# Optimization experiments

Hardware: AMD Instinct MI355X
Metric: run time of the kernel (lower is better)

Reference implementation:

```python
import jax, jax.numpy as jnp
import numpy as np

H = 128          # input spatial size forced by hardcoded reshape (8 * 16)
BATCH = 128
BLK = 8          # block_size
SUB = 16         # out_channels (sub-frames)
WIN = 3          # window


def setup_inputs() -> dict:
    key = jax.random.key(0)
    k1, k2 = jax.random.split(key, 2)
    coded = jax.random.normal(k1, (BATCH, 1, H, H), dtype=jnp.float32)
    # Conv3d weight: [out=16*64, in/groups=1, kD=9, 1, 1]; kaiming-like scale sqrt(2/9)
    weight = jax.random.normal(k2, (SUB * BLK * BLK, 1, WIN * WIN, 1, 1), dtype=jnp.float32) * np.sqrt(2.0 / 9.0).astype(np.float32)
    bias = jnp.zeros((SUB * BLK * BLK,), dtype=jnp.float32)
    return {"coded": coded, "weight": weight, "bias": bias}


def reference(coded, weight, bias):
    N = coded.shape[0]
    # --- window_shuffle: conv with 3x3 identity filters, pad 1 == 9 shifted copies ---
    pad = jnp.pad(coded, ((0, 0), (0, 0), (1, 1), (1, 1)))  # [N,1,H+2,H+2]
    patches = jnp.stack(
        [pad[:, 0, i:i + H, j:j + H] for i in range(WIN) for j in range(WIN)],
        axis=1,
    )  # [N,9,H,H]
    # --- reverse_pixel_shuffle (space-to-depth, block 8), vectorized over the 9 channels ---
    Hs = H // BLK  # 16
    x = patches.reshape(N, WIN * WIN, Hs, BLK, Hs, BLK)
    x = x.transpose(0, 1, 3, 5, 2, 4).reshape(N, WIN * WIN, BLK * BLK, Hs, Hs)
    x = x.transpose(0, 2, 1, 3, 4)  # [N,64,9,16,16] (torch.stack dim=2 order)
    # --- depthwise Conv3d: groups=64, kernel (9,1,1) -> per-group 9-tap dot ---
    W = weight.reshape(BLK * BLK, SUB, WIN * WIN)  # [64,16,9]
    b = bias.reshape(BLK * BLK, SUB)               # [64,16]
    out = jnp.einsum('ngihw,gmi->ngmhw', x, W) + b[None, :, :, None, None]  # [N,64,16,16,16]
    # --- reshape/transpose/pixel-shuffle ---
    out = out.transpose(0, 2, 1, 3, 4).reshape(N, SUB * BLK * BLK, Hs, Hs)  # [N,1024,16,16]
    out = out.reshape(N, SUB, BLK, BLK, Hs, Hs)
    out = out.transpose(0, 1, 4, 2, 5, 3).reshape(N, SUB, H, H)  # [N,16,128,128]
    return out
```

## Files before the change

### kernel.cpp

```cpp
#include <hip/hip_runtime.h>


#define H 128
#define N_BATCH 128
#define SUB 16

__global__ void wprep_kernel(const float* __restrict__ w,
                             const float* __restrict__ bias,
                             float* __restrict__ Wt) {
    int t = blockIdx.x * blockDim.x + threadIdx.x;
    if (t >= 8 * 16 * 8) return;
    int b1 = t >> 7;
    int m  = (t >> 3) & 15;
    int j  = t & 7;
    int oc = (b1 * 8 + j) * 16 + m;
    float* dst = Wt + (b1 * 16 + m) * 80;
#pragma unroll
    for (int i = 0; i < 9; ++i) dst[j * 9 + i] = w[oc * 9 + i];
    dst[72 + j] = bias[oc];
}

__global__ __launch_bounds__(256, 8) void shiftconv_kernel(
        const float* __restrict__ x,
        const float* __restrict__ Wt,
        float* __restrict__ out) {
    int bid = blockIdx.x;
    int nlo = bid & 7;
    int q   = bid >> 3;
    int mh  = q & 1;
    int rh  = (q >> 1) & 1;
    int b1  = (q >> 2) & 7;
    int n   = ((q >> 5) << 3) | nlo;

    __shared__ float ws[8 * 80];
    {
        int t = threadIdx.x;
        if (t < 160)
            ((float4*)ws)[t] = ((const float4*)(Wt + (b1 * 16 + mh * 8) * 80))[t];
    }

    int c  = threadIdx.x & 31;
    int r8 = threadIdx.x >> 5;
    int y  = b1 + (rh << 6) + (r8 << 3);
    int x0 = c << 2;
    int h  = c & 1;

    const float* xn = x + (size_t)n * (H * H);

    float in[3][6];
#pragma unroll
    for (int dy = 0; dy < 3; ++dy) {
        int ry = y + dy - 1;
        if (ry >= 0 && ry < H) {
            const float* row = xn + ry * H + x0;
            float4 a = *(const float4*)(row);
            in[dy][1] = a.x; in[dy][2] = a.y; in[dy][3] = a.z; in[dy][4] = a.w;
            in[dy][0] = (x0 > 0)     ? row[-1] : 0.0f;
            in[dy][5] = (x0 + 4 < H) ? row[4]  : 0.0f;
        } else {
#pragma unroll
            for (int k = 0; k < 6; ++k) in[dy][k] = 0.0f;
        }
    }

    __syncthreads();

    float* outbase = out + ((size_t)(n * SUB + mh * 8)) * (H * H) + y * H + x0;

#pragma unroll
    for (int mi = 0; mi < 8; ++mi) {
        const float* wb  = ws + mi * 80;
        const float* wpp = wb + h * 36;
        float acc[4];
#pragma unroll
        for (int j = 0; j < 4; ++j) acc[j] = wb[72 + 4 * h + j];
#pragma unroll
        for (int dy = 0; dy < 3; ++dy) {
#pragma unroll
            for (int dj = 0; dj < 3; ++dj) {
#pragma unroll
                for (int j = 0; j < 4; ++j) {
                    acc[j] = fmaf(in[dy][j + dj], wpp[j * 9 + dy * 3 + dj], acc[j]);
                }
            }
        }
        *(float4*)(outbase + (size_t)mi * (H * H)) =
            make_float4(acc[0], acc[1], acc[2], acc[3]);
    }
}

extern "C" void kernel_launch(void* const* d_in, const int* in_sizes, int n_in,
                              void* d_out, int out_size, void* d_ws, size_t ws_size,
                              hipStream_t stream) {
    const float* coded  = (const float*)d_in[0];
    const float* weight = (const float*)d_in[1];
    const float* bias   = (const float*)d_in[2];
    float* out = (float*)d_out;
    float* Wt  = (float*)d_ws;

    wprep_kernel<<<4, 256, 0, stream>>>(weight, bias, Wt);
    shiftconv_kernel<<<N_BATCH * 8 * 2 * 2, 256, 0, stream>>>(coded, Wt, out);
}
```

Measured before the change: 151.2 us.

## Fuse weight prep into conv kernel and keep weights in registers

Removes the separate weight-reorder kernel and has each block gather its weights and bias from global memory into shared memory. The thread mapping changes so each warp owns one output channel and keeps its 40 weights in registers while looping over 8 rows, instead of reading weights from shared memory per channel. Horizontal halo values now come from warp shuffles rather than extra scalar loads, and outputs are written with nontemporal stores. In exchange it uses more registers (launch bounds drop to 4 blocks per SM), reloads input rows once per channel-warp, and does uncoalesced strided weight gathers in every block.

```diff
diff --git a/kernel.cpp b/kernel.cpp
--- a/kernel.cpp
+++ b/kernel.cpp
@@ -5,24 +5,12 @@
 #define N_BATCH 128
 #define SUB 16
 
-__global__ void wprep_kernel(const float* __restrict__ w,
-                             const float* __restrict__ bias,
-                             float* __restrict__ Wt) {
-    int t = blockIdx.x * blockDim.x + threadIdx.x;
-    if (t >= 8 * 16 * 8) return;
-    int b1 = t >> 7;
-    int m  = (t >> 3) & 15;
-    int j  = t & 7;
-    int oc = (b1 * 8 + j) * 16 + m;
-    float* dst = Wt + (b1 * 16 + m) * 80;
-#pragma unroll
-    for (int i = 0; i < 9; ++i) dst[j * 9 + i] = w[oc * 9 + i];
-    dst[72 + j] = bias[oc];
-}
+typedef float floatx4 __attribute__((ext_vector_type(4)));
 
-__global__ __launch_bounds__(256, 8) void shiftconv_kernel(
+__global__ __launch_bounds__(256, 4) void shiftconv_kernel(
         const float* __restrict__ x,
-        const float* __restrict__ Wt,
+        const float* __restrict__ w,
+        const float* __restrict__ bias,
         float* __restrict__ out) {
     int bid = blockIdx.x;
     int nlo = bid & 7;
@@ -32,60 +20,70 @@
     int b1  = (q >> 2) & 7;
     int n   = ((q >> 5) << 3) | nlo;
 
-    __shared__ float ws[8 * 80];
+    __shared__ float ws[8 * 2 * 40];
     {
         int t = threadIdx.x;
-        if (t < 160)
-            ((float4*)ws)[t] = ((const float4*)(Wt + (b1 * 16 + mh * 8) * 80))[t];
+        if (t < 64) {
+            int ml = t >> 3, j = t & 7;
+            int oc = b1 * 128 + j * 16 + mh * 8 + ml;
+            float* dst = ws + (ml * 2 + (j >> 2)) * 40;
+            int j4 = j & 3;
+#pragma unroll
+            for (int i = 0; i < 9; ++i) dst[j4 * 9 + i] = w[oc * 9 + i];
+            dst[36 + j4] = bias[oc];
+        }
     }
+    __syncthreads();
 
     int c  = threadIdx.x & 31;
-    int r8 = threadIdx.x >> 5;
-    int y  = b1 + (rh << 6) + (r8 << 3);
+    int mq = threadIdx.x >> 5;
+    int h  = c & 1;
     int x0 = c << 2;
-    int h  = c & 1;
 
-    const float* xn = x + (size_t)n * (H * H);
-
-    float in[3][6];
+    float wr[40];
+    {
+        const float4* wp = (const float4*)(ws + (mq * 2 + h) * 40);
 #pragma unroll
-    for (int dy = 0; dy < 3; ++dy) {
-        int ry = y + dy - 1;
-        if (ry >= 0 && ry < H) {
-            const float* row = xn + ry * H + x0;
-            float4 a = *(const float4*)(row);
-            in[dy][1] = a.x; in[dy][2] = a.y; in[dy][3] = a.z; in[dy][4] = a.w;
-            in[dy][0] = (x0 > 0)     ? row[-1] : 0.0f;
-            in[dy][5] = (x0 + 4 < H) ? row[4]  : 0.0f;
-        } else {
-#pragma unroll
-            for (int k = 0; k < 6; ++k) in[dy][k] = 0.0f;
+        for (int k = 0; k < 10; ++k) {
+            float4 v = wp[k];
+            wr[4 * k]     = v.x;
+            wr[4 * k + 1] = v.y;
+            wr[4 * k + 2] = v.z;
+            wr[4 * k + 3] = v.w;
         }
     }
 
-    __syncthreads();
-
-    float* outbase = out + ((size_t)(n * SUB + mh * 8)) * (H * H) + y * H + x0;
+    const float* xn = x + (size_t)n * (H * H);
+    float* ob = out + ((size_t)(n * SUB + mh * 8 + mq)) * (H * H) + x0;
 
 #pragma unroll
-    for (int mi = 0; mi < 8; ++mi) {
-        const float* wb  = ws + mi * 80;
-        const float* wpp = wb + h * 36;
+    for (int r = 0; r < 8; ++r) {
+        int y = b1 + (rh << 6) + (r << 3);
+        float in[3][6];
+#pragma unroll
+        for (int dy = 0; dy < 3; ++dy) {
+            int ry = y + dy - 1;
+            float4 a = make_float4(0.f, 0.f, 0.f, 0.f);
+            if ((unsigned)ry < H)
+                a = *(const float4*)(xn + ry * H + x0);
+            in[dy][1] = a.x; in[dy][2] = a.y; in[dy][3] = a.z; in[dy][4] = a.w;
+            float lft = __shfl_up(a.w, 1);
+            float rgt = __shfl_down(a.x, 1);
+            in[dy][0] = (c > 0)  ? lft : 0.f;
+            in[dy][5] = (c < 31) ? rgt : 0.f;
+        }
         float acc[4];
 #pragma unroll
-        for (int j = 0; j < 4; ++j) acc[j] = wb[72 + 4 * h + j];
+        for (int j = 0; j < 4; ++j) acc[j] = wr[36 + j];
 #pragma unroll
-        for (int dy = 0; dy < 3; ++dy) {
+        for (int dy = 0; dy < 3; ++dy)
 #pragma unroll
-            for (int dj = 0; dj < 3; ++dj) {
+            for (int dj = 0; dj < 3; ++dj)
 #pragma unroll
-                for (int j = 0; j < 4; ++j) {
-                    acc[j] = fmaf(in[dy][j + dj], wpp[j * 9 + dy * 3 + dj], acc[j]);
-                }
-            }
-        }
-        *(float4*)(outbase + (size_t)mi * (H * H)) =
-            make_float4(acc[0], acc[1], acc[2], acc[3]);
+                for (int j = 0; j < 4; ++j)
+                    acc[j] = fmaf(in[dy][j + dj], wr[j * 9 + dy * 3 + dj], acc[j]);
+        floatx4 v = {acc[0], acc[1], acc[2], acc[3]};
+        __builtin_nontemporal_store(v, (floatx4*)(ob + y * H));
     }
 }
 
@@ -96,8 +94,6 @@
     const float* weight = (const float*)d_in[1];
     const float* bias   = (const float*)d_in[2];
     float* out = (float*)d_out;
-    float* Wt  = (float*)d_ws;
 
-    wprep_kernel<<<4, 256, 0, stream>>>(weight, bias, Wt);
-    shiftconv_kernel<<<N_BATCH * 8 * 2 * 2, 256, 0, stream>>>(coded, Wt, out);
+    shiftconv_kernel<<<N_BATCH * 8 * 2 * 2, 256, 0, stream>>>(coded, weight, bias, out);
 }
```

Result: slower. 172.2 us (+13.9%).
